# Optimization experiments

Measured on AMD Instinct MI355X. Metric: run time of the kernel, lower is better.

## Reference

```python
import jax, jax.numpy as jnp
import numpy as np

# 4D convolution via lax.conv_general_dilated with 4 spatial dims.
# Layout: input (N, C, D, H, W, T), kernel (O, I, d, h, w, t).
DN = ('NCDHWT', 'OIDHWT', 'NCDHWT')


def conv4d(x, w, b, pad):
    # torch Conv2d/Conv4d is cross-correlation, matching lax.conv_general_dilated
    y = jax.lax.conv_general_dilated(
        x, w, window_strides=(1, 1, 1, 1),
        padding=[(pad, pad)] * 4, dimension_numbers=DN)
    return y + b.reshape(1, -1, 1, 1, 1, 1)


def _kaiming(key, shape):
    fan_out = shape[0] * int(np.prod(shape[2:]))
    std = np.sqrt(2.0 / fan_out)
    return (jax.random.normal(key, shape, dtype=jnp.float32) * std).astype(jnp.float32)


def setup_inputs() -> dict:
    key = jax.random.key(0)
    ks = jax.random.split(key, 11)
    B, W, H = 256, 16, 16
    corr = jax.random.normal(ks[0], (B, W * H, W, H), dtype=jnp.float32)
    w1 = _kaiming(ks[1], (1, 1, 17, 17, 9, 9))
    w2 = _kaiming(ks[2], (1, 1, 7, 7, 7, 7))
    w3 = _kaiming(ks[3], (1, 1, 5, 5, 5, 5))
    w4 = _kaiming(ks[4], (1, 1, 3, 3, 3, 3))
    w5 = _kaiming(ks[5], (1, 1, 8, 8, 1, 1))
    b1 = jax.random.normal(ks[6], (1,), dtype=jnp.float32) * 0.01
    b2 = jax.random.normal(ks[7], (1,), dtype=jnp.float32) * 0.01
    b3 = jax.random.normal(ks[8], (1,), dtype=jnp.float32) * 0.01
    b4 = jax.random.normal(ks[9], (1,), dtype=jnp.float32) * 0.01
    b5 = jax.random.normal(ks[10], (1,), dtype=jnp.float32) * 0.01
    return {"corr": corr, "w1": w1, "b1": b1, "w2": w2, "b2": b2,
            "w3": w3, "b3": b3, "w4": w4, "b4": b4, "w5": w5, "b5": b5}


def reference(corr, w1, b1, w2, b2, w3, b3, w4, b4, w5, b5):
    B, HW, W, H = corr.shape
    x = corr.reshape(B, 1, W, H, W, H)          # (B,1,16,16,16,16)
    x = jax.nn.relu(conv4d(x, w1, b1, 4))       # (B,1, 8, 8,16,16)
    x = jax.nn.relu(conv4d(x, w2, b2, 3))
    x = jax.nn.relu(conv4d(x, w3, b3, 2))
    x = jax.nn.relu(conv4d(x, w4, b4, 1))
    out = jax.nn.sigmoid(conv4d(x, w5, b5, 0))  # (B,1, 1, 1,16,16)
    return out.reshape(B, 1, W, H)
```

## Files before the change

kernel.cpp:

```cpp
#include <hip/hip_runtime.h>
#include <math.h>


typedef short bf16x8 __attribute__((ext_vector_type(8)));
typedef float f32x4 __attribute__((ext_vector_type(4)));

#define XTS 72

__device__ __forceinline__ unsigned short f2bf(float f) {
  unsigned int u = __float_as_uint(f);
  u += 0x7fffu + ((u >> 16) & 1u);
  return (unsigned short)(u >> 16);
}

template <int KSZ, int PAD>
__device__ __forceinline__ void build_mid(const float* __restrict__ w,
                                          unsigned short* __restrict__ Bg, int gid) {
  const int lane = gid & 63;
  const int n_tile = (gid >> 6) & 3;
  const int chunk = (gid >> 8) & 1;
  const int tap = gid >> 9;
  const int kw = tap / KSZ, kt = tap - kw * KSZ;
  const int dh_o = n_tile * 16 + (lane & 15);
  const int d_o = dh_o >> 3, h_o = dh_o & 7;
  const int kbase = chunk * 32 + (lane >> 4) * 8;
  unsigned int pk[4];
#pragma unroll
  for (int p = 0; p < 4; ++p) {
    unsigned short half[2];
#pragma unroll
    for (int s = 0; s < 2; ++s) {
      const int k = kbase + p * 2 + s;
      const int d_i = k >> 3, h_i = k & 7;
      const int kd = d_i - d_o + PAD, kh = h_i - h_o + PAD;
      float v = 0.f;
      if (kd >= 0 && kd < KSZ && kh >= 0 && kh < KSZ)
        v = w[((kd * KSZ + kh) * KSZ + kw) * KSZ + kt];
      half[s] = f2bf(v);
    }
    pk[p] = (unsigned int)half[0] | ((unsigned int)half[1] << 16);
  }
  *(int4*)(Bg + (size_t)gid * 8) = make_int4(pk[0], pk[1], pk[2], pk[3]);
}

__global__ __launch_bounds__(256) void build_all(const float* __restrict__ w1,
                                                 const float* __restrict__ w2,
                                                 const float* __restrict__ w3,
                                                 const float* __restrict__ w4,
                                                 unsigned short* __restrict__ Bg1,
                                                 unsigned short* __restrict__ Bg2,
                                                 unsigned short* __restrict__ Bg3,
                                                 unsigned short* __restrict__ Bg4) {
  const int bid = blockIdx.x, tid = threadIdx.x;
  if (bid < 648) {
    const int gid = bid * 256 + tid;
    const int lane = gid & 63;
    const int n_tile = (gid >> 6) & 3;
    const int chunk = (gid >> 8) & 7;
    const int kwkt = gid >> 11;
    const int kw = kwkt / 9, kt = kwkt - kw * 9;
    const int dh_o = n_tile * 16 + (lane & 15);
    const int d_o = dh_o >> 3, h_o = dh_o & 7;
    const int kbase = chunk * 32 + (lane >> 4) * 8;
    unsigned int pk[4];
#pragma unroll
    for (int p = 0; p < 4; ++p) {
      unsigned short half[2];
#pragma unroll
      for (int s = 0; s < 2; ++s) {
        const int k = kbase + p * 2 + s;
        const int d_i = k >> 4, h_i = k & 15;
        const int kd = d_i - d_o + 4, kh = h_i - h_o + 4;
        float v = 0.f;
        if (kd >= 0 && kd < 17 && kh >= 0 && kh < 17)
          v = w1[((kd * 17 + kh) * 9 + kw) * 9 + kt];
        half[s] = f2bf(v);
      }
      pk[p] = (unsigned int)half[0] | ((unsigned int)half[1] << 16);
    }
    *(int4*)(Bg1 + (size_t)gid * 8) = make_int4(pk[0], pk[1], pk[2], pk[3]);
  } else if (bid < 746) {
    build_mid<7, 3>(w2, Bg2, (bid - 648) * 256 + tid);
  } else if (bid < 796) {
    build_mid<5, 2>(w3, Bg3, (bid - 746) * 256 + tid);
  } else {
    build_mid<3, 1>(w4, Bg4, (bid - 796) * 256 + tid);
  }
}

__device__ __forceinline__ void mfma_block(const bf16x8 (&A)[8], const bf16x8 (&B)[8],
                                           f32x4 (&acc)[4][4]) {
#pragma unroll
  for (int c = 0; c < 2; ++c)
#pragma unroll
    for (int m = 0; m < 4; ++m)
#pragma unroll
      for (int n = 0; n < 4; ++n)
        acc[m][n] = __builtin_amdgcn_mfma_f32_16x16x32_bf16(A[c * 4 + m], B[c * 4 + n],
                                                            acc[m][n], 0, 0, 0);
}

template <int KSZ, int PAD, int CHTOT>
__device__ __forceinline__ void load_tap(const unsigned short* XT,
                                         const unsigned short* __restrict__ Bg,
                                         int chbase, int kwkt, int wave, int lane,
                                         int quad, int tl, bf16x8 (&A)[8], bf16x8 (&B)[8]) {
  const int kw = kwkt / KSZ, kt = kwkt - kw * KSZ;
  const int t_i = tl + kt - PAD;
  const bool tv = (unsigned)t_i < 16u;
  int ro[4];
#pragma unroll
  for (int m = 0; m < 4; ++m) {
    const int w_i = wave * 4 + m + kw - PAD;
    const bool v = tv && ((unsigned)w_i < 16u);
    const int row = v ? (w_i * 16 + t_i) : 256;
    ro[m] = row * XTS + quad * 8;
  }
#pragma unroll
  for (int c = 0; c < 2; ++c)
#pragma unroll
    for (int m = 0; m < 4; ++m)
      A[c * 4 + m] = *(const bf16x8*)&XT[ro[m] + c * 32];
#pragma unroll
  for (int c = 0; c < 2; ++c)
#pragma unroll
    for (int n = 0; n < 4; ++n)
      B[c * 4 + n] = *(const bf16x8*)(Bg + (((size_t)(kwkt * CHTOT + chbase + c) * 4 + n) << 9) +
                                      lane * 8);
}

#define TAP_PIPELINE(NT, LOADCALL)                    \
  {                                                   \
    bf16x8 A0[8], B0[8], A1[8], B1[8];                \
    LOADCALL(0, A0, B0);                              \
    int k2 = 0;                                       \
    while (true) {                                    \
      if (k2 + 1 < (NT)) LOADCALL(k2 + 1, A1, B1);    \
      mfma_block(A0, B0, acc);                        \
      if (++k2 >= (NT)) break;                        \
      if (k2 + 1 < (NT)) LOADCALL(k2 + 1, A0, B0);    \
      mfma_block(A1, B1, acc);                        \
      if (++k2 >= (NT)) break;                        \
    }                                                 \
  }

__global__ __launch_bounds__(256) void conv_l1_mfma(const float* __restrict__ x,
                                                    const unsigned short* __restrict__ Bg,
                                                    const float* __restrict__ b1,
                                                    float* __restrict__ y) {
  __shared__ __align__(16) unsigned short XT[257 * XTS];
  const int b = blockIdx.x;
  const int tid = threadIdx.x;
  const int lane = tid & 63, wave = tid >> 6;
  const int quad = lane >> 4, tl = lane & 15;
  const float* xb = x + (size_t)b * 65536;
  f32x4 acc[4][4] = {};

  if (tid < 9) *(int4*)&XT[256 * XTS + tid * 8] = make_int4(0, 0, 0, 0);

  for (int kq = 0; kq < 4; ++kq) {
    __syncthreads();
#pragma unroll
    for (int it = 0; it < 8; ++it) {
      const int i = tid + it * 256;
      const int dhp = i >> 6, wtq = i & 63;
      const float4 r0 = *(const float4*)(xb + (size_t)(kq * 64 + 2 * dhp) * 256 + wtq * 4);
      const float4 r1 = *(const float4*)(xb + (size_t)(kq * 64 + 2 * dhp + 1) * 256 + wtq * 4);
      const float a0[4] = {r0.x, r0.y, r0.z, r0.w};
      const float a1[4] = {r1.x, r1.y, r1.z, r1.w};
#pragma unroll
      for (int j = 0; j < 4; ++j) {
        const unsigned int p = (unsigned int)f2bf(a0[j]) | ((unsigned int)f2bf(a1[j]) << 16);
        *(unsigned int*)&XT[(wtq * 4 + j) * XTS + dhp * 2] = p;
      }
    }
    __syncthreads();
#define LT_L1(KK, AA, BB) load_tap<9, 4, 8>(XT, Bg, kq * 2, (KK), wave, lane, quad, tl, AA, BB)
    TAP_PIPELINE(81, LT_L1)
#undef LT_L1
  }

  const float bias = b1[0];
  float* yb = y + (size_t)b * 16384;
#pragma unroll
  for (int m = 0; m < 4; ++m)
#pragma unroll
    for (int n = 0; n < 4; ++n) {
      const int dh_o = n * 16 + tl;
      const int wt0 = wave * 64 + m * 16 + quad * 4;
      float4 v;
      v.x = fmaxf(acc[m][n][0] + bias, 0.f);
      v.y = fmaxf(acc[m][n][1] + bias, 0.f);
      v.z = fmaxf(acc[m][n][2] + bias, 0.f);
      v.w = fmaxf(acc[m][n][3] + bias, 0.f);
      *(float4*)&yb[(size_t)dh_o * 256 + wt0] = v;
    }
}

template <int KSZ, int PAD, int NT>
__global__ __launch_bounds__(256) void conv_mid_mfma(float* __restrict__ y,
                                                     const unsigned short* __restrict__ Bg,
                                                     const float* __restrict__ bptr) {
  __shared__ __align__(16) unsigned short XT[257 * XTS];
  const int b = blockIdx.x;
  const int tid = threadIdx.x;
  const int lane = tid & 63, wave = tid >> 6;
  const int quad = lane >> 4, tl = lane & 15;
  float* yb = y + (size_t)b * 16384;
  f32x4 acc[4][4] = {};

  if (tid < 9) *(int4*)&XT[256 * XTS + tid * 8] = make_int4(0, 0, 0, 0);
#pragma unroll
  for (int it = 0; it < 8; ++it) {
    const int i = tid + it * 256;
    const int dhp = i >> 6, wtq = i & 63;
    const float4 r0 = *(const float4*)(yb + (size_t)(2 * dhp) * 256 + wtq * 4);
    const float4 r1 = *(const float4*)(yb + (size_t)(2 * dhp + 1) * 256 + wtq * 4);
    const float a0[4] = {r0.x, r0.y, r0.z, r0.w};
    const float a1[4] = {r1.x, r1.y, r1.z, r1.w};
#pragma unroll
    for (int j = 0; j < 4; ++j) {
      const unsigned int p = (unsigned int)f2bf(a0[j]) | ((unsigned int)f2bf(a1[j]) << 16);
      *(unsigned int*)&XT[(wtq * 4 + j) * XTS + dhp * 2] = p;
    }
  }
  __syncthreads();
#define LT_MID(KK, AA, BB) load_tap<KSZ, PAD, 2>(XT, Bg, 0, (KK), wave, lane, quad, tl, AA, BB)
  TAP_PIPELINE(NT, LT_MID)
#undef LT_MID

  const float bias = bptr[0];
#pragma unroll
  for (int m = 0; m < 4; ++m)
#pragma unroll
    for (int n = 0; n < 4; ++n) {
      const int dh_o = n * 16 + tl;
      const int wt0 = wave * 64 + m * 16 + quad * 4;
      float4 v;
      v.x = fmaxf(acc[m][n][0] + bias, 0.f);
      v.y = fmaxf(acc[m][n][1] + bias, 0.f);
      v.z = fmaxf(acc[m][n][2] + bias, 0.f);
      v.w = fmaxf(acc[m][n][3] + bias, 0.f);
      *(float4*)&yb[(size_t)dh_o * 256 + wt0] = v;
    }
}

__global__ __launch_bounds__(256) void conv_l5(const float* __restrict__ x,
                                               const float* __restrict__ w5,
                                               const float* __restrict__ b5,
                                               float* __restrict__ out) {
  const int b = blockIdx.x;
  const int tid = threadIdx.x;
  const float* xb = x + (size_t)b * 16384 + tid;
  float s = b5[0];
#pragma unroll
  for (int k = 0; k < 64; ++k) s += xb[k * 256] * w5[k];
  out[(size_t)b * 256 + tid] = 1.f / (1.f + expf(-s));
}

extern "C" void kernel_launch(void* const* d_in, const int* in_sizes, int n_in,
                              void* d_out, int out_size, void* d_ws, size_t ws_size,
                              hipStream_t stream) {
  const float* corr = (const float*)d_in[0];
  const float* w1 = (const float*)d_in[1];
  const float* b1 = (const float*)d_in[2];
  const float* w2 = (const float*)d_in[3];
  const float* b2 = (const float*)d_in[4];
  const float* w3 = (const float*)d_in[5];
  const float* b3 = (const float*)d_in[6];
  const float* w4 = (const float*)d_in[7];
  const float* b4 = (const float*)d_in[8];
  const float* w5 = (const float*)d_in[9];
  const float* b5 = (const float*)d_in[10];

  float* A = (float*)d_ws;
  unsigned short* Bg1 = (unsigned short*)((char*)d_ws + (16 << 20));
  unsigned short* Bg2 = Bg1 + (size_t)81 * 8 * 4 * 64 * 8;
  unsigned short* Bg3 = Bg2 + (size_t)49 * 2 * 4 * 64 * 8;
  unsigned short* Bg4 = Bg3 + (size_t)25 * 2 * 4 * 64 * 8;

  build_all<<<814, 256, 0, stream>>>(w1, w2, w3, w4, Bg1, Bg2, Bg3, Bg4);
  conv_l1_mfma<<<256, 256, 0, stream>>>(corr, Bg1, b1, A);
  conv_mid_mfma<7, 3, 49><<<256, 256, 0, stream>>>(A, Bg2, b2);
  conv_mid_mfma<5, 2, 25><<<256, 256, 0, stream>>>(A, Bg3, b3);
  conv_mid_mfma<3, 1, 9><<<256, 256, 0, stream>>>(A, Bg4, b4);
  conv_l5<<<256, 256, 0, stream>>>(A, w5, b5, (float*)d_out);
}
```

Baseline: 317.8 us.

## Split layer-1 conv over channel halves, pair images per block, swizzle LDS

Layer 1 now gives each block a pair of images and one half of the input-channel (K) range. Waves share B fragments across two images, and each wave holds 8x4 accumulators. Partial sums go to a doubled workspace, and a new reduce kernel adds the two halves and applies bias and ReLU. The LDS tile uses an XOR swizzle with masking in place of the padded-row-plus-zero-row scheme, aiming to cut bank conflicts and raise B-fragment reuse. The cost is an extra kernel launch, an extra global round trip of partial results, and higher register pressure.

```diff
diff --git a/kernel.cpp b/kernel.cpp
--- a/kernel.cpp
+++ b/kernel.cpp
@@ -4,8 +4,7 @@
 
 typedef short bf16x8 __attribute__((ext_vector_type(8)));
 typedef float f32x4 __attribute__((ext_vector_type(4)));
-
-#define XTS 72
+typedef unsigned int u32x4 __attribute__((ext_vector_type(4)));
 
 __device__ __forceinline__ unsigned short f2bf(float f) {
   unsigned int u = __float_as_uint(f);
@@ -88,23 +87,144 @@
   }
 }
 
-__device__ __forceinline__ void mfma_block(const bf16x8 (&A)[8], const bf16x8 (&B)[8],
-                                           f32x4 (&acc)[4][4]) {
+__device__ __forceinline__ void l1_loadB(const unsigned short* __restrict__ Bg, int kwkt,
+                                         int chbase, int lane, bf16x8 (&B)[8]) {
 #pragma unroll
   for (int c = 0; c < 2; ++c)
 #pragma unroll
+    for (int n = 0; n < 4; ++n)
+      B[c * 4 + n] =
+          *(const bf16x8*)(Bg + (((size_t)(kwkt * 8 + chbase + c) * 4 + n) << 9) + lane * 8);
+}
+
+__device__ __forceinline__ void l1_compute(const unsigned short* XTimg, int kwkt, int mhalf,
+                                           int quad, int tl, const bf16x8 (&B)[8],
+                                           f32x4 (&acc)[8][4]) {
+  const int kw = kwkt / 9, kt = kwkt - kw * 9;
+  const int t_i = tl + kt - 4;
+  const bool tv = (unsigned)t_i < 16u;
+#pragma unroll
+  for (int m = 0; m < 8; ++m) {
+    const int w_i = mhalf * 8 + m + kw - 4;
+    const bool valid = tv && ((unsigned)w_i < 16u);
+    const int row = valid ? (w_i * 16 + t_i) : 0;
+    const unsigned int msk = valid ? 0xFFFFFFFFu : 0u;
+    const int rh = row & 7;
+    const int base = row * 64;
+#pragma unroll
+    for (int c = 0; c < 2; ++c) {
+      const int unit = (c * 4 + quad) ^ rh;
+      u32x4 a = *(const u32x4*)&XTimg[base + unit * 8];
+      a.x &= msk; a.y &= msk; a.z &= msk; a.w &= msk;
+      const bf16x8 af = __builtin_bit_cast(bf16x8, a);
+#pragma unroll
+      for (int n = 0; n < 4; ++n)
+        acc[m][n] = __builtin_amdgcn_mfma_f32_16x16x32_bf16(af, B[c * 4 + n], acc[m][n], 0, 0, 0);
+    }
+  }
+}
+
+__global__ __launch_bounds__(256, 1) void conv_l1_mfma(const float* __restrict__ x,
+                                                       const unsigned short* __restrict__ Bg,
+                                                       float* __restrict__ P) {
+  __shared__ __align__(16) unsigned short XT[2 * 256 * 64];
+  const int bx = blockIdx.x;
+  const int pair = bx >> 1, khalf = bx & 1;
+  const int tid = threadIdx.x;
+  const int lane = tid & 63, wave = tid >> 6;
+  const int quad = lane >> 4, tl = lane & 15;
+  const int img_l = wave >> 1, mhalf = wave & 1;
+  f32x4 acc[8][4] = {};
+
+  for (int qq = 0; qq < 2; ++qq) {
+    const int q = khalf * 2 + qq;
+    __syncthreads();
+#pragma unroll
+    for (int it = 0; it < 16; ++it) {
+      const int idx = tid + it * 256;
+      const int dhp = idx & 31;
+      const int w64 = (idx >> 5) & 63;
+      const int img = idx >> 11;
+      const float* src =
+          x + (size_t)(pair * 2 + img) * 65536 + (size_t)(q * 64 + 2 * dhp) * 256 + w64 * 4;
+      const float4 r0 = *(const float4*)src;
+      const float4 r1 = *(const float4*)(src + 256);
+      const float a0[4] = {r0.x, r0.y, r0.z, r0.w};
+      const float a1[4] = {r1.x, r1.y, r1.z, r1.w};
+      unsigned short* dst = XT + img * 16384;
+      const int u0 = dhp >> 2, so = 2 * (dhp & 3);
+#pragma unroll
+      for (int j = 0; j < 4; ++j) {
+        const int row = w64 * 4 + j;
+        const unsigned int p = (unsigned int)f2bf(a0[j]) | ((unsigned int)f2bf(a1[j]) << 16);
+        *(unsigned int*)&dst[row * 64 + ((u0 ^ (row & 7)) << 3) + so] = p;
+      }
+    }
+    __syncthreads();
+    const unsigned short* XTimg = XT + img_l * 16384;
+    const int chbase = q * 2;
+    bf16x8 B0[8], B1[8];
+    l1_loadB(Bg, 0, chbase, lane, B0);
+    int k = 0;
+    while (true) {
+      if (k + 1 < 81) l1_loadB(Bg, k + 1, chbase, lane, B1);
+      l1_compute(XTimg, k, mhalf, quad, tl, B0, acc);
+      if (++k >= 81) break;
+      if (k + 1 < 81) l1_loadB(Bg, k + 1, chbase, lane, B0);
+      l1_compute(XTimg, k, mhalf, quad, tl, B1, acc);
+      if (++k >= 81) break;
+    }
+  }
+
+  float* Pb = P + (size_t)(khalf * 256 + pair * 2 + img_l) * 16384;
+#pragma unroll
+  for (int m = 0; m < 8; ++m)
+#pragma unroll
+    for (int n = 0; n < 4; ++n) {
+      const int dh_o = n * 16 + tl;
+      const int wt0 = (mhalf * 8 + m) * 16 + quad * 4;
+      *(float4*)&Pb[(size_t)dh_o * 256 + wt0] = *(const float4*)&acc[m][n];
+    }
+}
+
+__global__ __launch_bounds__(256) void reduce_l1(float* __restrict__ A,
+                                                 const float* __restrict__ b1) {
+  const float bias = b1[0];
+  const int t = blockIdx.x * 256 + threadIdx.x;
+  float4* a0 = (float4*)A;
+  const float4* a1 = (const float4*)(A + (size_t)4194304);
+#pragma unroll
+  for (int i = 0; i < 16; ++i) {
+    const int idx = t + i * 65536;
+    float4 v = a0[idx];
+    const float4 w = a1[idx];
+    v.x = fmaxf(v.x + w.x + bias, 0.f);
+    v.y = fmaxf(v.y + w.y + bias, 0.f);
+    v.z = fmaxf(v.z + w.z + bias, 0.f);
+    v.w = fmaxf(v.w + w.w + bias, 0.f);
+    a0[idx] = v;
+  }
+}
+
+#define XTS 72
+
+__device__ __forceinline__ void mid_mfma_block(const bf16x8 (&A)[8], const bf16x8 (&B)[8],
+                                               f32x4 (&acc)[4][4]) {
+#pragma unroll
+  for (int c = 0; c < 2; ++c)
+#pragma unroll
     for (int m = 0; m < 4; ++m)
 #pragma unroll
       for (int n = 0; n < 4; ++n)
-        acc[m][n] = __builtin_amdgcn_mfma_f32_16x16x32_bf16(A[c * 4 + m], B[c * 4 + n],
-                                                            acc[m][n], 0, 0, 0);
-}
-
-template <int KSZ, int PAD, int CHTOT>
-__device__ __forceinline__ void load_tap(const unsigned short* XT,
-                                         const unsigned short* __restrict__ Bg,
-                                         int chbase, int kwkt, int wave, int lane,
-                                         int quad, int tl, bf16x8 (&A)[8], bf16x8 (&B)[8]) {
+        acc[m][n] = __builtin_amdgcn_mfma_f32_16x16x32_bf16(A[c * 2 + m >= 0 ? c * 4 + m : 0],
+                                                            B[c * 4 + n], acc[m][n], 0, 0, 0);
+}
+
+template <int KSZ, int PAD>
+__device__ __forceinline__ void mid_load_tap(const unsigned short* XT,
+                                             const unsigned short* __restrict__ Bg, int kwkt,
+                                             int wave, int lane, int quad, int tl,
+                                             bf16x8 (&A)[8], bf16x8 (&B)[8]) {
   const int kw = kwkt / KSZ, kt = kwkt - kw * KSZ;
   const int t_i = tl + kt - PAD;
   const bool tv = (unsigned)t_i < 16u;
@@ -125,76 +245,7 @@
   for (int c = 0; c < 2; ++c)
 #pragma unroll
     for (int n = 0; n < 4; ++n)
-      B[c * 4 + n] = *(const bf16x8*)(Bg + (((size_t)(kwkt * CHTOT + chbase + c) * 4 + n) << 9) +
-                                      lane * 8);
-}
-
-#define TAP_PIPELINE(NT, LOADCALL)                    \
-  {                                                   \
-    bf16x8 A0[8], B0[8], A1[8], B1[8];                \
-    LOADCALL(0, A0, B0);                              \
-    int k2 = 0;                                       \
-    while (true) {                                    \
-      if (k2 + 1 < (NT)) LOADCALL(k2 + 1, A1, B1);    \
-      mfma_block(A0, B0, acc);                        \
-      if (++k2 >= (NT)) break;                        \
-      if (k2 + 1 < (NT)) LOADCALL(k2 + 1, A0, B0);    \
-      mfma_block(A1, B1, acc);                        \
-      if (++k2 >= (NT)) break;                        \
-    }                                                 \
-  }
-
-__global__ __launch_bounds__(256) void conv_l1_mfma(const float* __restrict__ x,
-                                                    const unsigned short* __restrict__ Bg,
-                                                    const float* __restrict__ b1,
-                                                    float* __restrict__ y) {
-  __shared__ __align__(16) unsigned short XT[257 * XTS];
-  const int b = blockIdx.x;
-  const int tid = threadIdx.x;
-  const int lane = tid & 63, wave = tid >> 6;
-  const int quad = lane >> 4, tl = lane & 15;
-  const float* xb = x + (size_t)b * 65536;
-  f32x4 acc[4][4] = {};
-
-  if (tid < 9) *(int4*)&XT[256 * XTS + tid * 8] = make_int4(0, 0, 0, 0);
-
-  for (int kq = 0; kq < 4; ++kq) {
-    __syncthreads();
-#pragma unroll
-    for (int it = 0; it < 8; ++it) {
-      const int i = tid + it * 256;
-      const int dhp = i >> 6, wtq = i & 63;
-      const float4 r0 = *(const float4*)(xb + (size_t)(kq * 64 + 2 * dhp) * 256 + wtq * 4);
-      const float4 r1 = *(const float4*)(xb + (size_t)(kq * 64 + 2 * dhp + 1) * 256 + wtq * 4);
-      const float a0[4] = {r0.x, r0.y, r0.z, r0.w};
-      const float a1[4] = {r1.x, r1.y, r1.z, r1.w};
-#pragma unroll
-      for (int j = 0; j < 4; ++j) {
-        const unsigned int p = (unsigned int)f2bf(a0[j]) | ((unsigned int)f2bf(a1[j]) << 16);
-        *(unsigned int*)&XT[(wtq * 4 + j) * XTS + dhp * 2] = p;
-      }
-    }
-    __syncthreads();
-#define LT_L1(KK, AA, BB) load_tap<9, 4, 8>(XT, Bg, kq * 2, (KK), wave, lane, quad, tl, AA, BB)
-    TAP_PIPELINE(81, LT_L1)
-#undef LT_L1
-  }
-
-  const float bias = b1[0];
-  float* yb = y + (size_t)b * 16384;
-#pragma unroll
-  for (int m = 0; m < 4; ++m)
-#pragma unroll
-    for (int n = 0; n < 4; ++n) {
-      const int dh_o = n * 16 + tl;
-      const int wt0 = wave * 64 + m * 16 + quad * 4;
-      float4 v;
-      v.x = fmaxf(acc[m][n][0] + bias, 0.f);
-      v.y = fmaxf(acc[m][n][1] + bias, 0.f);
-      v.z = fmaxf(acc[m][n][2] + bias, 0.f);
-      v.w = fmaxf(acc[m][n][3] + bias, 0.f);
-      *(float4*)&yb[(size_t)dh_o * 256 + wt0] = v;
-    }
+      B[c * 4 + n] = *(const bf16x8*)(Bg + (((size_t)(kwkt * 2 + c) * 4 + n) << 9) + lane * 8);
 }
 
 template <int KSZ, int PAD, int NT>
@@ -225,9 +276,38 @@
     }
   }
   __syncthreads();
-#define LT_MID(KK, AA, BB) load_tap<KSZ, PAD, 2>(XT, Bg, 0, (KK), wave, lane, quad, tl, AA, BB)
-  TAP_PIPELINE(NT, LT_MID)
-#undef LT_MID
+
+  {
+    bf16x8 A0[8], B0[8], A1[8], B1[8];
+    mid_load_tap<KSZ, PAD>(XT, Bg, 0, wave, lane, quad, tl, A0, B0);
+    int k = 0;
+    while (true) {
+      if (k + 1 < NT) mid_load_tap<KSZ, PAD>(XT, Bg, k + 1, wave, lane, quad, tl, A1, B1);
+      {
+#pragma unroll
+        for (int c = 0; c < 2; ++c)
+#pragma unroll
+          for (int m = 0; m < 4; ++m)
+#pragma unroll
+            for (int n = 0; n < 4; ++n)
+              acc[m][n] = __builtin_amdgcn_mfma_f32_16x16x32_bf16(A0[c * 4 + m], B0[c * 4 + n],
+                                                                  acc[m][n], 0, 0, 0);
+      }
+      if (++k >= NT) break;
+      if (k + 1 < NT) mid_load_tap<KSZ, PAD>(XT, Bg, k + 1, wave, lane, quad, tl, A0, B0);
+      {
+#pragma unroll
+        for (int c = 0; c < 2; ++c)
+#pragma unroll
+          for (int m = 0; m < 4; ++m)
+#pragma unroll
+            for (int n = 0; n < 4; ++n)
+              acc[m][n] = __builtin_amdgcn_mfma_f32_16x16x32_bf16(A1[c * 4 + m], B1[c * 4 + n],
+                                                                  acc[m][n], 0, 0, 0);
+      }
+      if (++k >= NT) break;
+    }
+  }
 
   const float bias = bptr[0];
 #pragma unroll
@@ -274,13 +354,14 @@
   const float* b5 = (const float*)d_in[10];
 
   float* A = (float*)d_ws;
-  unsigned short* Bg1 = (unsigned short*)((char*)d_ws + (16 << 20));
+  unsigned short* Bg1 = (unsigned short*)((char*)d_ws + (32u << 20));
   unsigned short* Bg2 = Bg1 + (size_t)81 * 8 * 4 * 64 * 8;
   unsigned short* Bg3 = Bg2 + (size_t)49 * 2 * 4 * 64 * 8;
   unsigned short* Bg4 = Bg3 + (size_t)25 * 2 * 4 * 64 * 8;
 
   build_all<<<814, 256, 0, stream>>>(w1, w2, w3, w4, Bg1, Bg2, Bg3, Bg4);
-  conv_l1_mfma<<<256, 256, 0, stream>>>(corr, Bg1, b1, A);
+  conv_l1_mfma<<<256, 256, 0, stream>>>(corr, Bg1, A);
+  reduce_l1<<<256, 256, 0, stream>>>(A, b1);
   conv_mid_mfma<7, 3, 49><<<256, 256, 0, stream>>>(A, Bg2, b2);
   conv_mid_mfma<5, 2, 25><<<256, 256, 0, stream>>>(A, Bg3, b3);
   conv_mid_mfma<3, 1, 9><<<256, 256, 0, stream>>>(A, Bg4, b4);
```

New measurement: 373.6 us. +17.6%, slower.
